# Performance work log

Measured on AMD Instinct MI355X. Metric: run time of the kernel, lower is better.

## Reference

```python
import jax, jax.numpy as jnp
import numpy as np

B, S, D, H = 2, 2048, 1024, 16
DK = D // H
NEG = -1e9


def setup_inputs() -> dict:
    key = jax.random.key(0)
    ks = jax.random.split(key, 12)
    inp = {
        "query": jax.random.normal(ks[0], (B, S, D), jnp.float32),
        "key": jax.random.normal(ks[1], (B, S, D), jnp.float32),
        "value": jax.random.normal(ks[2], (B, S, D), jnp.float32),
        "mask": jax.random.randint(ks[3], (B, S), 0, 2, jnp.int32),
    }
    # 4 linears (q, k, v, out), each d_model x d_model with bias.
    scale = 1.0 / np.sqrt(D)
    for i, name in enumerate(["wq", "wk", "wv", "wo"]):
        inp[name] = jax.random.uniform(ks[4 + i], (D, D), jnp.float32, -scale, scale)
        inp["b" + name[1]] = jax.random.uniform(ks[8 + i], (D,), jnp.float32, -scale, scale)
    return inp


def _split_heads(x):  # [B,S,D] -> [B,H,S,DK]
    return x.reshape(B, S, H, DK).transpose(0, 2, 1, 3)


def reference(query, key, value, mask, wq, bq, wk, bk, wv, bv, wo, bo):
    q = _split_heads(query @ wq.T + bq)
    k = _split_heads(key @ wk.T + bk)
    v = _split_heads(value @ wv.T + bv)
    scores = jnp.einsum("bhqd,bhkd->bhqk", q, k) / jnp.sqrt(jnp.float32(DK))
    # mask: [B,S] -> [B,1,1,S]; masked_fill where mask == 0
    m = mask[:, None, None, :]
    scores = jnp.where(m == 0, NEG, scores)
    attn = jax.nn.softmax(scores, axis=-1)  # dropout p=0 (eval) -> identity
    x = jnp.einsum("bhqk,bhkd->bhqd", attn, v)
    x = x.transpose(0, 2, 1, 3).reshape(B, S, D)
    return x @ wo.T + bo
```

## Files before the change

kernel.cpp:

```cpp
#include <hip/hip_runtime.h>


typedef _Float16 f16;
typedef _Float16 f16x8 __attribute__((ext_vector_type(8)));
typedef _Float16 f16x4 __attribute__((ext_vector_type(4)));
typedef float f32x4 __attribute__((ext_vector_type(4)));

#define MFMA_F16(a, b, c) __builtin_amdgcn_mfma_f32_16x16x32_f16((a), (b), (c), 0, 0, 0)
#define MFMA16(a, b, c) __builtin_amdgcn_mfma_f32_16x16x16f16((a), (b), (c), 0, 0, 0)
#define L2E 1.44269504088896340736f

__device__ __forceinline__ void gld16(const void* g, void* l) {
    __builtin_amdgcn_global_load_lds(
        (__attribute__((address_space(1))) void*)(g),
        (__attribute__((address_space(3))) void*)(l), 16, 0, 0);
}

__global__ __launch_bounds__(256) void cvt_kernel(
    const float* __restrict__ q, const float* __restrict__ k,
    const float* __restrict__ v,
    const float* __restrict__ wq, const float* __restrict__ wk,
    const float* __restrict__ wv, const float* __restrict__ wo,
    f16* __restrict__ oq, f16* __restrict__ ok, f16* __restrict__ ov,
    f16* __restrict__ owq, f16* __restrict__ owk, f16* __restrict__ owv,
    f16* __restrict__ owo)
{
    const int z = blockIdx.y;
    const float* src;
    f16* dst;
    int n;
    switch (z) {
        case 0: src = q;  dst = oq;  n = 4194304; break;
        case 1: src = k;  dst = ok;  n = 4194304; break;
        case 2: src = v;  dst = ov;  n = 4194304; break;
        case 3: src = wq; dst = owq; n = 1048576; break;
        case 4: src = wk; dst = owk; n = 1048576; break;
        case 5: src = wv; dst = owv; n = 1048576; break;
        default: src = wo; dst = owo; n = 1048576; break;
    }
    int idx = (blockIdx.x * 256 + threadIdx.x) * 8;
    if (idx >= n) return;
    float4 a = *(const float4*)(src + idx);
    float4 b = *(const float4*)(src + idx + 4);
    f16x8 h = { (f16)a.x, (f16)a.y, (f16)a.z, (f16)a.w,
                (f16)b.x, (f16)b.y, (f16)b.z, (f16)b.w };
    *(f16x8*)(dst + idx) = h;
}

__global__ __launch_bounds__(256) void proj_qkv_kernel(
    const f16* __restrict__ xq, const f16* __restrict__ xk,
    const f16* __restrict__ xv,
    const f16* __restrict__ wqh, const f16* __restrict__ wkh,
    const f16* __restrict__ wvh,
    const float* __restrict__ bq, const float* __restrict__ bk,
    const float* __restrict__ bv,
    f16* __restrict__ qh, f16* __restrict__ kh, f16* __restrict__ vt)
{
    const int z = blockIdx.z;
    const f16* X = (z == 0) ? xq : (z == 1) ? xk : xv;
    const f16* W = (z == 0) ? wqh : (z == 1) ? wkh : wvh;
    const float* bias = (z == 0) ? bq : (z == 1) ? bk : bv;
    const f16* P0 = (z < 2) ? W : X;
    const f16* P1 = (z < 2) ? X : W;

    __shared__ __align__(16) f16 As[128 * 64];
    __shared__ __align__(16) f16 Bs[128 * 64];

    const int t = threadIdx.x;
    const int wave = t >> 6, lane = t & 63, quad = lane >> 4, l15 = lane & 15;
    const int m_base = (wave >> 1) * 64, n_base = (wave & 1) * 64;
    const int blockM = (z < 2) ? blockIdx.y * 128 : blockIdx.x * 128;
    const int blockN = (z < 2) ? blockIdx.x * 128 : blockIdx.y * 128;

    const int srow = lane >> 3;
    const int sblk = (lane & 7) ^ srow;

    f32x4 acc[4][4];
#pragma unroll
    for (int mt = 0; mt < 4; mt++)
#pragma unroll
        for (int nt = 0; nt < 4; nt++)
            acc[mt][nt] = (f32x4){0.f, 0.f, 0.f, 0.f};

    for (int k0 = 0; k0 < 1024; k0 += 64) {
        __syncthreads();
#pragma unroll
        for (int j = 0; j < 4; j++) {
            int r0 = wave * 32 + j * 8;
            gld16(&P0[(size_t)(blockM + r0 + srow) * 1024 + k0 + sblk * 8],
                  &As[r0 * 64]);
            gld16(&P1[(size_t)(blockN + r0 + srow) * 1024 + k0 + sblk * 8],
                  &Bs[r0 * 64]);
        }
        __syncthreads();

#pragma unroll
        for (int c = 0; c < 2; c++) {
            f16x8 af[4], bf[4];
#pragma unroll
            for (int mt = 0; mt < 4; mt++)
                af[mt] = *(const f16x8*)(&As[(m_base + mt * 16 + l15) * 64 +
                                             (((c * 4 + quad) ^ (l15 & 7)) << 3)]);
#pragma unroll
            for (int nt = 0; nt < 4; nt++)
                bf[nt] = *(const f16x8*)(&Bs[(n_base + nt * 16 + l15) * 64 +
                                             (((c * 4 + quad) ^ (l15 & 7)) << 3)]);
#pragma unroll
            for (int mt = 0; mt < 4; mt++)
#pragma unroll
                for (int nt = 0; nt < 4; nt++)
                    acc[mt][nt] = MFMA_F16(af[mt], bf[nt], acc[mt][nt]);
        }
    }

    if (z < 2) {
        f16* o = (z == 0) ? qh : kh;
        const float scale = (z == 0) ? 0.125f * L2E : 1.0f;
#pragma unroll
        for (int mt = 0; mt < 4; mt++) {
            int j0 = blockM + m_base + mt * 16 + quad * 4;
            float4 b4 = *(const float4*)(&bias[j0]);
            int h = j0 >> 6, dk = j0 & 63;
#pragma unroll
            for (int nt = 0; nt < 4; nt++) {
                int s_g = blockN + n_base + nt * 16 + l15;
                int b = s_g >> 11, s = s_g & 2047;
                f16x4 pk = { (f16)((acc[mt][nt][0] + b4.x) * scale),
                             (f16)((acc[mt][nt][1] + b4.y) * scale),
                             (f16)((acc[mt][nt][2] + b4.z) * scale),
                             (f16)((acc[mt][nt][3] + b4.w) * scale) };
                *(f16x4*)(&o[(((size_t)(b * 16 + h) * 2048 + s) << 6) + dk]) = pk;
            }
        }
    } else {
        float bv_[4];
#pragma unroll
        for (int nt = 0; nt < 4; nt++)
            bv_[nt] = bias[blockN + n_base + nt * 16 + l15];
#pragma unroll
        for (int mt = 0; mt < 4; mt++) {
            int row0 = blockM + m_base + mt * 16 + quad * 4;
            int b = row0 >> 11, s0 = row0 & 2047;
#pragma unroll
            for (int nt = 0; nt < 4; nt++) {
                int col_g = blockN + n_base + nt * 16 + l15;
                int h = col_g >> 6, dk = col_g & 63;
                f16x4 pk = { (f16)(acc[mt][nt][0] + bv_[nt]),
                             (f16)(acc[mt][nt][1] + bv_[nt]),
                             (f16)(acc[mt][nt][2] + bv_[nt]),
                             (f16)(acc[mt][nt][3] + bv_[nt]) };
                *(f16x4*)(&vt[((size_t)((b * 16 + h) * 64 + dk) << 11) + s0]) = pk;
            }
        }
    }
}

__global__ __launch_bounds__(256) void flash_kernel(
    const f16* __restrict__ qh, const f16* __restrict__ kh,
    const f16* __restrict__ vt, const int* __restrict__ mask,
    f16* __restrict__ ctx)
{
    __shared__ __align__(16) f16 Ks[64 * 64];
    __shared__ __align__(16) f16 Vts[64 * 64];
    __shared__ float bias_all[2048];

    const int t = threadIdx.x;
    const int wave = t >> 6, lane = t & 63, quad = lane >> 4, l15 = lane & 15;
    const int bh = blockIdx.x;
    const int b = bh >> 4, h = bh & 15;
    const int q0 = blockIdx.y * 128;

    const f16* qbase = qh + (size_t)bh * (2048 * 64);
    const f16* kbase = kh + (size_t)bh * (2048 * 64);
    const f16* vbase = vt + (size_t)bh * (64 * 2048);

#pragma unroll
    for (int j = 0; j < 8; j++) {
        int i = j * 256 + t;
        bias_all[i] = (mask[b * 2048 + i] == 0) ? -1.0e9f : 0.0f;
    }

    f16x8 qf[2][2];
#pragma unroll
    for (int cb = 0; cb < 2; cb++) {
        int qrow = q0 + wave * 32 + cb * 16 + l15;
        qf[cb][0] = *(const f16x8*)(&qbase[qrow * 64 + quad * 8]);
        qf[cb][1] = *(const f16x8*)(&qbase[qrow * 64 + 32 + quad * 8]);
    }

    f32x4 O[2][4];
#pragma unroll
    for (int cb = 0; cb < 2; cb++)
#pragma unroll
        for (int n = 0; n < 4; n++) O[cb][n] = (f32x4){0.f, 0.f, 0.f, 0.f};
    float l_part[2] = {0.f, 0.f};

    const int srow8 = lane >> 3;
    const int sblk = (lane & 7) ^ srow8;

    for (int kt = 0; kt < 32; kt++) {
        __syncthreads();
        const int key0 = kt * 64;
#pragma unroll
        for (int p = 0; p < 2; p++) {
            int r0 = p * 32 + wave * 8;
            int row = r0 + srow8;
            gld16(&kbase[(size_t)(key0 + row) * 64 + sblk * 8], &Ks[r0 * 64]);
            gld16(&vbase[(size_t)row * 2048 + key0 + sblk * 8], &Vts[r0 * 64]);
        }
        __syncthreads();

        f32x4 sc[2][4];
#pragma unroll
        for (int nt = 0; nt < 4; nt++) {
            const f16* krow = &Ks[(nt * 16 + l15) * 64];
            f16x8 kf0 = *(const f16x8*)(&krow[(quad ^ (l15 & 7)) << 3]);
            f16x8 kf1 = *(const f16x8*)(&krow[((quad + 4) ^ (l15 & 7)) << 3]);
            float4 b4 = *(const float4*)(&bias_all[key0 + nt * 16 + quad * 4]);
#pragma unroll
            for (int cb = 0; cb < 2; cb++) {
                f32x4 z4 = (f32x4){b4.x, b4.y, b4.z, b4.w};
                z4 = MFMA_F16(kf0, qf[cb][0], z4);
                sc[cb][nt] = MFMA_F16(kf1, qf[cb][1], z4);
            }
        }

        f16x4 pf[2][4];
#pragma unroll
        for (int cb = 0; cb < 2; cb++) {
            float rs = 0.f;
#pragma unroll
            for (int nt = 0; nt < 4; nt++)
#pragma unroll
                for (int i = 0; i < 4; i++) {
                    float p = exp2f(sc[cb][nt][i]);
                    rs += p;
                    pf[cb][nt][i] = (f16)p;
                }
            l_part[cb] += rs;
        }

#pragma unroll
        for (int nto = 0; nto < 4; nto++) {
            const f16* vrow = &Vts[(nto * 16 + l15) * 64];
#pragma unroll
            for (int nt = 0; nt < 4; nt++) {
                f16x4 vf = *(const f16x4*)(&vrow[
                    (((nt * 2 + (quad >> 1)) ^ (l15 & 7)) << 3) + (quad & 1) * 4]);
                O[0][nto] = MFMA16(vf, pf[0][nt], O[0][nto]);
                O[1][nto] = MFMA16(vf, pf[1][nt], O[1][nto]);
            }
        }
    }

#pragma unroll
    for (int cb = 0; cb < 2; cb++) {
        float l = l_part[cb];
        l += __shfl_xor(l, 16);
        l += __shfl_xor(l, 32);
        const float inv_l = 1.0f / l;
        int qrow = q0 + wave * 32 + cb * 16 + l15;
#pragma unroll
        for (int nto = 0; nto < 4; nto++) {
            f16x4 pk = { (f16)(O[cb][nto][0] * inv_l),
                         (f16)(O[cb][nto][1] * inv_l),
                         (f16)(O[cb][nto][2] * inv_l),
                         (f16)(O[cb][nto][3] * inv_l) };
            *(f16x4*)(&ctx[(size_t)(b * 2048 + qrow) * 1024 + h * 64 +
                           nto * 16 + quad * 4]) = pk;
        }
    }
}

__global__ __launch_bounds__(256) void proj_out_kernel(
    const f16* __restrict__ ctx, const f16* __restrict__ woh,
    const float* __restrict__ bo, float* __restrict__ out)
{
    __shared__ __align__(16) f16 As[128 * 64];
    __shared__ __align__(16) f16 Bs[128 * 64];

    const int t = threadIdx.x;
    const int wave = t >> 6, lane = t & 63, quad = lane >> 4, l15 = lane & 15;
    const int m_base = (wave >> 1) * 64, n_base = (wave & 1) * 64;
    const int blockM = blockIdx.x * 128;
    const int blockN = blockIdx.y * 128;

    const int srow = lane >> 3;
    const int sblk = (lane & 7) ^ srow;

    f32x4 acc[4][4];
#pragma unroll
    for (int mt = 0; mt < 4; mt++)
#pragma unroll
        for (int nt = 0; nt < 4; nt++)
            acc[mt][nt] = (f32x4){0.f, 0.f, 0.f, 0.f};

    for (int k0 = 0; k0 < 1024; k0 += 64) {
        __syncthreads();
#pragma unroll
        for (int j = 0; j < 4; j++) {
            int r0 = wave * 32 + j * 8;
            gld16(&ctx[(size_t)(blockM + r0 + srow) * 1024 + k0 + sblk * 8],
                  &As[r0 * 64]);
            gld16(&woh[(size_t)(blockN + r0 + srow) * 1024 + k0 + sblk * 8],
                  &Bs[r0 * 64]);
        }
        __syncthreads();

#pragma unroll
        for (int c = 0; c < 2; c++) {
            f16x8 af[4], bf[4];
#pragma unroll
            for (int mt = 0; mt < 4; mt++)
                af[mt] = *(const f16x8*)(&As[(m_base + mt * 16 + l15) * 64 +
                                             (((c * 4 + quad) ^ (l15 & 7)) << 3)]);
#pragma unroll
            for (int nt = 0; nt < 4; nt++)
                bf[nt] = *(const f16x8*)(&Bs[(n_base + nt * 16 + l15) * 64 +
                                             (((c * 4 + quad) ^ (l15 & 7)) << 3)]);
#pragma unroll
            for (int mt = 0; mt < 4; mt++)
#pragma unroll
                for (int nt = 0; nt < 4; nt++)
                    acc[mt][nt] = MFMA_F16(af[mt], bf[nt], acc[mt][nt]);
        }
    }

    float bo_[4];
#pragma unroll
    for (int nt = 0; nt < 4; nt++)
        bo_[nt] = bo[blockN + n_base + nt * 16 + l15];

#pragma unroll
    for (int mt = 0; mt < 4; mt++) {
        int row0 = blockM + m_base + mt * 16 + quad * 4;
#pragma unroll
        for (int nt = 0; nt < 4; nt++) {
            int col_g = blockN + n_base + nt * 16 + l15;
#pragma unroll
            for (int i = 0; i < 4; i++)
                out[(size_t)(row0 + i) * 1024 + col_g] = acc[mt][nt][i] + bo_[nt];
        }
    }
}

extern "C" void kernel_launch(void* const* d_in, const int* in_sizes, int n_in,
                              void* d_out, int out_size, void* d_ws, size_t ws_size,
                              hipStream_t stream) {
    const float* query = (const float*)d_in[0];
    const float* key_  = (const float*)d_in[1];
    const float* value = (const float*)d_in[2];
    const int*   mask  = (const int*)d_in[3];
    const float* wq = (const float*)d_in[4];
    const float* bq = (const float*)d_in[5];
    const float* wk = (const float*)d_in[6];
    const float* bk = (const float*)d_in[7];
    const float* wv = (const float*)d_in[8];
    const float* bv = (const float*)d_in[9];
    const float* wo = (const float*)d_in[10];
    const float* bo = (const float*)d_in[11];
    float* out = (float*)d_out;

    f16* xq  = (f16*)d_ws;
    f16* xk  = xq  + 4194304;
    f16* xv  = xk  + 4194304;
    f16* wqh = xv  + 4194304;
    f16* wkh = wqh + 1048576;
    f16* wvh = wkh + 1048576;
    f16* woh = wvh + 1048576;
    f16* qh  = woh + 1048576;
    f16* kh  = qh  + 4194304;
    f16* vt  = kh  + 4194304;
    f16* ctx = xq;

    cvt_kernel<<<dim3(2048, 7), 256, 0, stream>>>(
        query, key_, value, wq, wk, wv, wo, xq, xk, xv, wqh, wkh, wvh, woh);
    proj_qkv_kernel<<<dim3(32, 8, 3), 256, 0, stream>>>(
        xq, xk, xv, wqh, wkh, wvh, bq, bk, bv, qh, kh, vt);
    flash_kernel<<<dim3(32, 16), 256, 0, stream>>>(qh, kh, vt, mask, ctx);
    proj_out_kernel<<<dim3(32, 8), 256, 0, stream>>>(ctx, woh, bo, out);
}
```

Baseline: 242.3 us.

## Double-buffer K/V and GEMM tiles in LDS, shrink out-proj N tile

Both the flash attention kernel and the output projection now ping-pong two LDS buffers. The next K/V (or A/B) tile is issued through direct global-to-LDS loads before computing on the current tile, with one barrier per iteration instead of two. This is meant to hide global load latency behind the MFMA work. The output projection tile drops from 128x128 to 128x64, doubling the grid to improve occupancy and load balance. Softmax probabilities are packed to f16 with cvt_pkrtz, which truncates instead of rounding to nearest. Overlap depends on the compiler not inserting a full vmcnt wait before the LDS reads.

```diff
diff --git a/kernel.cpp b/kernel.cpp
--- a/kernel.cpp
+++ b/kernel.cpp
@@ -4,7 +4,10 @@
 typedef _Float16 f16;
 typedef _Float16 f16x8 __attribute__((ext_vector_type(8)));
 typedef _Float16 f16x4 __attribute__((ext_vector_type(4)));
+typedef __fp16 fp16x2r __attribute__((ext_vector_type(2)));
 typedef float f32x4 __attribute__((ext_vector_type(4)));
+
+union F16x4u { f16x4 v; fp16x2r h[2]; };
 
 #define MFMA_F16(a, b, c) __builtin_amdgcn_mfma_f32_16x16x32_f16((a), (b), (c), 0, 0, 0)
 #define MFMA16(a, b, c) __builtin_amdgcn_mfma_f32_16x16x16f16((a), (b), (c), 0, 0, 0)
@@ -160,8 +163,8 @@
     const f16* __restrict__ vt, const int* __restrict__ mask,
     f16* __restrict__ ctx)
 {
-    __shared__ __align__(16) f16 Ks[64 * 64];
-    __shared__ __align__(16) f16 Vts[64 * 64];
+    __shared__ __align__(16) f16 Ks[2][64 * 64];
+    __shared__ __align__(16) f16 Vts[2][64 * 64];
     __shared__ float bias_all[2048];
 
     const int t = threadIdx.x;
@@ -198,22 +201,36 @@
     const int srow8 = lane >> 3;
     const int sblk = (lane & 7) ^ srow8;
 
+#pragma unroll
+    for (int p = 0; p < 2; p++) {
+        int r0 = p * 32 + wave * 8;
+        int row = r0 + srow8;
+        gld16(&kbase[(size_t)row * 64 + sblk * 8], &Ks[0][r0 * 64]);
+        gld16(&vbase[(size_t)row * 2048 + sblk * 8], &Vts[0][r0 * 64]);
+    }
+
     for (int kt = 0; kt < 32; kt++) {
+        const int cur = kt & 1;
         __syncthreads();
+
+        if (kt < 31) {
+            const int key0n = (kt + 1) * 64;
+#pragma unroll
+            for (int p = 0; p < 2; p++) {
+                int r0 = p * 32 + wave * 8;
+                int row = r0 + srow8;
+                gld16(&kbase[(size_t)(key0n + row) * 64 + sblk * 8],
+                      &Ks[cur ^ 1][r0 * 64]);
+                gld16(&vbase[(size_t)row * 2048 + key0n + sblk * 8],
+                      &Vts[cur ^ 1][r0 * 64]);
+            }
+        }
+
         const int key0 = kt * 64;
-#pragma unroll
-        for (int p = 0; p < 2; p++) {
-            int r0 = p * 32 + wave * 8;
-            int row = r0 + srow8;
-            gld16(&kbase[(size_t)(key0 + row) * 64 + sblk * 8], &Ks[r0 * 64]);
-            gld16(&vbase[(size_t)row * 2048 + key0 + sblk * 8], &Vts[r0 * 64]);
-        }
-        __syncthreads();
-
         f32x4 sc[2][4];
 #pragma unroll
         for (int nt = 0; nt < 4; nt++) {
-            const f16* krow = &Ks[(nt * 16 + l15) * 64];
+            const f16* krow = &Ks[cur][(nt * 16 + l15) * 64];
             f16x8 kf0 = *(const f16x8*)(&krow[(quad ^ (l15 & 7)) << 3]);
             f16x8 kf1 = *(const f16x8*)(&krow[((quad + 4) ^ (l15 & 7)) << 3]);
             float4 b4 = *(const float4*)(&bias_all[key0 + nt * 16 + quad * 4]);
@@ -230,19 +247,23 @@
         for (int cb = 0; cb < 2; cb++) {
             float rs = 0.f;
 #pragma unroll
-            for (int nt = 0; nt < 4; nt++)
-#pragma unroll
-                for (int i = 0; i < 4; i++) {
-                    float p = exp2f(sc[cb][nt][i]);
-                    rs += p;
-                    pf[cb][nt][i] = (f16)p;
-                }
+            for (int nt = 0; nt < 4; nt++) {
+                float p0 = exp2f(sc[cb][nt][0]);
+                float p1 = exp2f(sc[cb][nt][1]);
+                float p2 = exp2f(sc[cb][nt][2]);
+                float p3 = exp2f(sc[cb][nt][3]);
+                rs += (p0 + p1) + (p2 + p3);
+                F16x4u u;
+                u.h[0] = __builtin_amdgcn_cvt_pkrtz(p0, p1);
+                u.h[1] = __builtin_amdgcn_cvt_pkrtz(p2, p3);
+                pf[cb][nt] = u.v;
+            }
             l_part[cb] += rs;
         }
 
 #pragma unroll
         for (int nto = 0; nto < 4; nto++) {
-            const f16* vrow = &Vts[(nto * 16 + l15) * 64];
+            const f16* vrow = &Vts[cur][(nto * 16 + l15) * 64];
 #pragma unroll
             for (int nt = 0; nt < 4; nt++) {
                 f16x4 vf = *(const f16x4*)(&vrow[
@@ -276,66 +297,87 @@
     const f16* __restrict__ ctx, const f16* __restrict__ woh,
     const float* __restrict__ bo, float* __restrict__ out)
 {
-    __shared__ __align__(16) f16 As[128 * 64];
-    __shared__ __align__(16) f16 Bs[128 * 64];
+    __shared__ __align__(16) f16 As[2][128 * 64];
+    __shared__ __align__(16) f16 Bs[2][64 * 64];
 
     const int t = threadIdx.x;
     const int wave = t >> 6, lane = t & 63, quad = lane >> 4, l15 = lane & 15;
-    const int m_base = (wave >> 1) * 64, n_base = (wave & 1) * 64;
+    const int m_base = (wave >> 1) * 64, n_base = (wave & 1) * 32;
     const int blockM = blockIdx.x * 128;
-    const int blockN = blockIdx.y * 128;
+    const int blockN = blockIdx.y * 64;
 
     const int srow = lane >> 3;
     const int sblk = (lane & 7) ^ srow;
 
-    f32x4 acc[4][4];
+    f32x4 acc[4][2];
 #pragma unroll
     for (int mt = 0; mt < 4; mt++)
 #pragma unroll
-        for (int nt = 0; nt < 4; nt++)
+        for (int nt = 0; nt < 2; nt++)
             acc[mt][nt] = (f32x4){0.f, 0.f, 0.f, 0.f};
 
-    for (int k0 = 0; k0 < 1024; k0 += 64) {
+#pragma unroll
+    for (int j = 0; j < 4; j++) {
+        int r0 = wave * 32 + j * 8;
+        gld16(&ctx[(size_t)(blockM + r0 + srow) * 1024 + sblk * 8],
+              &As[0][r0 * 64]);
+    }
+#pragma unroll
+    for (int j = 0; j < 2; j++) {
+        int r0 = wave * 16 + j * 8;
+        gld16(&woh[(size_t)(blockN + r0 + srow) * 1024 + sblk * 8],
+              &Bs[0][r0 * 64]);
+    }
+
+    for (int ki = 0; ki < 16; ki++) {
+        const int cur = ki & 1;
         __syncthreads();
-#pragma unroll
-        for (int j = 0; j < 4; j++) {
-            int r0 = wave * 32 + j * 8;
-            gld16(&ctx[(size_t)(blockM + r0 + srow) * 1024 + k0 + sblk * 8],
-                  &As[r0 * 64]);
-            gld16(&woh[(size_t)(blockN + r0 + srow) * 1024 + k0 + sblk * 8],
-                  &Bs[r0 * 64]);
-        }
-        __syncthreads();
+
+        if (ki < 15) {
+            const int k0n = (ki + 1) * 64;
+#pragma unroll
+            for (int j = 0; j < 4; j++) {
+                int r0 = wave * 32 + j * 8;
+                gld16(&ctx[(size_t)(blockM + r0 + srow) * 1024 + k0n + sblk * 8],
+                      &As[cur ^ 1][r0 * 64]);
+            }
+#pragma unroll
+            for (int j = 0; j < 2; j++) {
+                int r0 = wave * 16 + j * 8;
+                gld16(&woh[(size_t)(blockN + r0 + srow) * 1024 + k0n + sblk * 8],
+                      &Bs[cur ^ 1][r0 * 64]);
+            }
+        }
 
 #pragma unroll
         for (int c = 0; c < 2; c++) {
-            f16x8 af[4], bf[4];
+            f16x8 af[4], bf[2];
 #pragma unroll
             for (int mt = 0; mt < 4; mt++)
-                af[mt] = *(const f16x8*)(&As[(m_base + mt * 16 + l15) * 64 +
-                                             (((c * 4 + quad) ^ (l15 & 7)) << 3)]);
-#pragma unroll
-            for (int nt = 0; nt < 4; nt++)
-                bf[nt] = *(const f16x8*)(&Bs[(n_base + nt * 16 + l15) * 64 +
-                                             (((c * 4 + quad) ^ (l15 & 7)) << 3)]);
+                af[mt] = *(const f16x8*)(&As[cur][(m_base + mt * 16 + l15) * 64 +
+                                              (((c * 4 + quad) ^ (l15 & 7)) << 3)]);
+#pragma unroll
+            for (int nt = 0; nt < 2; nt++)
+                bf[nt] = *(const f16x8*)(&Bs[cur][(n_base + nt * 16 + l15) * 64 +
+                                              (((c * 4 + quad) ^ (l15 & 7)) << 3)]);
 #pragma unroll
             for (int mt = 0; mt < 4; mt++)
 #pragma unroll
-                for (int nt = 0; nt < 4; nt++)
+                for (int nt = 0; nt < 2; nt++)
                     acc[mt][nt] = MFMA_F16(af[mt], bf[nt], acc[mt][nt]);
         }
     }
 
-    float bo_[4];
-#pragma unroll
-    for (int nt = 0; nt < 4; nt++)
+    float bo_[2];
+#pragma unroll
+    for (int nt = 0; nt < 2; nt++)
         bo_[nt] = bo[blockN + n_base + nt * 16 + l15];
 
 #pragma unroll
     for (int mt = 0; mt < 4; mt++) {
         int row0 = blockM + m_base + mt * 16 + quad * 4;
 #pragma unroll
-        for (int nt = 0; nt < 4; nt++) {
+        for (int nt = 0; nt < 2; nt++) {
             int col_g = blockN + n_base + nt * 16 + l15;
 #pragma unroll
             for (int i = 0; i < 4; i++)
@@ -378,5 +420,5 @@
     proj_qkv_kernel<<<dim3(32, 8, 3), 256, 0, stream>>>(
         xq, xk, xv, wqh, wkh, wvh, bq, bk, bv, qh, kh, vt);
     flash_kernel<<<dim3(32, 16), 256, 0, stream>>>(qh, kh, vt, mask, ctx);
-    proj_out_kernel<<<dim3(32, 8), 256, 0, stream>>>(ctx, woh, bo, out);
-}
+    proj_out_kernel<<<dim3(32, 16), 256, 0, stream>>>(ctx, woh, bo, out);
+}
```

Measured after the change: 242.4 us. About the same (+0.0%).
